# Performance work log

Measured on AMD Instinct MI355X. Metric: run time of the kernel, lower is better.

## Reference

```python
import jax, jax.numpy as jnp
import numpy as np

B, T, E, H, D_PRICE = 16, 2048, 128, 4, 512


def setup_inputs() -> dict:
    key = jax.random.key(0)
    ks = jax.random.split(key, 22)
    f32 = jnp.float32

    def w(k, shape):
        fan_in = shape[0]
        return (jax.random.normal(k, shape, f32) / np.sqrt(fan_in)).astype(f32)

    def b(k, n):
        return (jax.random.normal(k, (n,), f32) * 0.01).astype(f32)

    inp = {
        # OHLC prices, positive, normalized scale
        "ohlc": jax.random.uniform(ks[0], (B, T, 4), f32, 0.5, 1.5),
        # ohlc_proj: Linear(4, 64)
        "Wp": w(ks[1], (4, 64)), "bp": b(ks[2], 64),
        # curvature_net: Linear(64,128) -> ReLU -> Linear(128,32)
        "Wc1": w(ks[3], (64, 128)), "bc1": b(ks[4], 128),
        "Wc2": w(ks[5], (128, 32)), "bc2": b(ks[6], 32),
        # volatility_net: Linear(64,64) -> ReLU -> Linear(64,16)
        "Wv1": w(ks[7], (64, 64)), "bv1": b(ks[8], 64),
        "Wv2": w(ks[9], (64, 16)), "bv2": b(ks[10], 16),
        # sr_field_net: Linear(64,64) -> ReLU -> Linear(64,16)
        "Ws1": w(ks[11], (64, 64)), "bs1": b(ks[12], 64),
        "Ws2": w(ks[13], (64, 16)), "bs2": b(ks[14], 16),
        # MultiheadAttention(embed_dim=128, num_heads=4): fused in-proj + out-proj
        "Wqkv": w(ks[15], (E, 3 * E)), "bqkv": b(ks[16], 3 * E),
        "Wo": w(ks[17], (E, E)), "bo": b(ks[18], E),
        # output_proj: Linear(128, d_price)
        "Wout": w(ks[19], (E, D_PRICE)), "bout": b(ks[20], D_PRICE),
    }
    return inp


def _mlp(x, W1, b1, W2, b2):
    return jax.nn.relu(x @ W1 + b1) @ W2 + b2


def reference(ohlc, Wp, bp, Wc1, bc1, Wc2, bc2, Wv1, bv1, Wv2, bv2,
              Ws1, bs1, Ws2, bs2, Wqkv, bqkv, Wo, bo, Wout, bout):
    # NB: compute_curvature / compute_volatility_surface / detect_sr_levels
    # in the original forward are dead code (results never used), so they are
    # omitted here; output math is identical.
    e = ohlc @ Wp + bp                                   # [B,T,64]
    feats = jnp.concatenate([
        e,
        _mlp(e, Wc1, bc1, Wc2, bc2),                     # [B,T,32]
        _mlp(e, Wv1, bv1, Wv2, bv2),                     # [B,T,16]
        _mlp(e, Ws1, bs1, Ws2, bs2),                     # [B,T,16]
    ], axis=-1)                                          # [B,T,128]

    Bn, Tn, En = feats.shape
    dh = En // H
    qkv = feats @ Wqkv + bqkv                            # [B,T,3E]
    q, k, v = jnp.split(qkv, 3, axis=-1)

    def heads(x):
        return x.reshape(Bn, Tn, H, dh).transpose(0, 2, 1, 3)  # [B,H,T,dh]

    q, k, v = heads(q), heads(k), heads(v)
    scores = jnp.einsum('bhqd,bhkd->bhqk', q, k) / np.sqrt(dh).astype(feats.dtype)
    a = jax.nn.softmax(scores, axis=-1)                  # [B,H,T,T]
    o = jnp.einsum('bhqk,bhkd->bhqd', a, v)
    o = o.transpose(0, 2, 1, 3).reshape(Bn, Tn, En)
    attended = o @ Wo + bo                               # [B,T,128]

    pooled = attended.mean(axis=1)                       # [B,128]
    return pooled @ Wout + bout                          # [B,512]
```

## Files before the change

### kernel.cpp

```cpp
#include <hip/hip_runtime.h>


typedef __attribute__((ext_vector_type(4)))  float f32x4;
typedef __attribute__((ext_vector_type(4)))  short short4v;
typedef __attribute__((ext_vector_type(8)))  short short8v;

static __device__ __forceinline__ unsigned short f2b(float f) {
    unsigned int u = __builtin_bit_cast(unsigned int, f);
    u += 0x7fffu + ((u >> 16) & 1u);
    return (unsigned short)(u >> 16);
}

static __device__ __forceinline__ unsigned int cvtpk_bf16(float a, float b) {
    unsigned int r;
    asm volatile("v_cvt_pk_bf16_f32 %0, %1, %2" : "=v"(r) : "v"(a), "v"(b));
    return r;
}

__global__ __launch_bounds__(256) void prep_kernel(
    const float* Wqkv, const float* Wc1, const float* Wc2, const float* Wv1,
    const float* Wv2, const float* Ws1, const float* Ws2,
    unsigned short* wqkvt, unsigned short* wc1t, unsigned short* wc2t,
    unsigned short* wv1t, unsigned short* wv2t, unsigned short* ws1t,
    unsigned short* ws2t, float* pooled, float* qkmax)
{
    int tid = threadIdx.x;
    if (blockIdx.x < 48) {
        __shared__ float tile[32][33];
        int bidn = blockIdx.x % 12, bidk = blockIdx.x / 12;
        int n0 = bidn * 32, k0 = bidk * 32;
        {
            int r = tid >> 3, cq = tid & 7;
            float4 v = *(const float4*)(Wqkv + (size_t)(k0 + r) * 384 + n0 + cq * 4);
            tile[r][cq*4+0] = v.x; tile[r][cq*4+1] = v.y;
            tile[r][cq*4+2] = v.z; tile[r][cq*4+3] = v.w;
        }
        __syncthreads();
        {
            int nr = tid >> 3, kq = tid & 7;
            union { unsigned short us[4]; short4v v; } pk;
#pragma unroll
            for (int j = 0; j < 4; ++j) pk.us[j] = f2b(tile[kq*4+j][nr]);
            *(short4v*)(wqkvt + (size_t)(n0 + nr) * 128 + k0 + kq * 4) = pk.v;
        }
        return;
    }
    int idx = (blockIdx.x - 48) * 256 + tid;
    if (idx < 8192)  { int n = idx >> 6, kk = idx & 63;  wc1t[idx] = f2b(Wc1[kk*128 + n]); return; }
    idx -= 8192;
    if (idx < 4096)  { int n = idx >> 7, kk = idx & 127; wc2t[idx] = f2b(Wc2[kk*32  + n]); return; }
    idx -= 4096;
    if (idx < 4096)  { int n = idx >> 6, kk = idx & 63;  wv1t[idx] = f2b(Wv1[kk*64  + n]); return; }
    idx -= 4096;
    if (idx < 1024)  { int n = idx >> 6, kk = idx & 63;  wv2t[idx] = f2b(Wv2[kk*16  + n]); return; }
    idx -= 1024;
    if (idx < 4096)  { int n = idx >> 6, kk = idx & 63;  ws1t[idx] = f2b(Ws1[kk*64  + n]); return; }
    idx -= 4096;
    if (idx < 1024)  { int n = idx >> 6, kk = idx & 63;  ws2t[idx] = f2b(Ws2[kk*16  + n]); return; }
    idx -= 1024;
    if (idx < 2048)  { pooled[idx] = 0.f; return; }
    idx -= 2048;
    if (idx < 128)   qkmax[idx] = 0.f;
}

template<int N, int K, int A_ROWB, int D_ROWB, bool RELU, bool TO_LDS>
static __device__ __forceinline__ void tile_gemm(
    const char* As, const unsigned short* __restrict__ BT,
    const float* __restrict__ bias, char* dst,
    unsigned short* __restrict__ gOut, int ocol,
    int m0, int w, int lane)
{
    constexpr int ASL = A_ROWB / 16, DSL = D_ROWB / 16;
    constexpr int NT = N / 16, KS = K / 32;
    int l15 = lane & 15, hi4 = lane >> 4;
    f32x4 acc[NT];
#pragma unroll
    for (int nt = 0; nt < NT; ++nt)
#pragma unroll
        for (int r = 0; r < 4; ++r) acc[nt][r] = 0.f;

#pragma unroll
    for (int ks = 0; ks < KS; ++ks) {
        int slot = ks * 4 + hi4;
        int m = w * 16 + l15;
        short8v af = *(const short8v*)(As + m * A_ROWB + ((slot ^ (m & (ASL - 1))) << 4));
#pragma unroll
        for (int nt = 0; nt < NT; ++nt) {
            int n = nt * 16 + l15;
            short8v bf = *(const short8v*)(BT + (size_t)n * K + slot * 8);
            acc[nt] = __builtin_amdgcn_mfma_f32_16x16x32_bf16(af, bf, acc[nt], 0, 0, 0);
        }
    }
#pragma unroll
    for (int nt = 0; nt < NT; ++nt) {
        int n = nt * 16 + l15;
        float bv = bias[n];
#pragma unroll
        for (int r = 0; r < 4; ++r) {
            int m = w * 16 + hi4 * 4 + r;
            float v = acc[nt][r] + bv;
            if (RELU) v = fmaxf(v, 0.f);
            if (TO_LDS) {
                int col = n;
                *(unsigned short*)(dst + m * D_ROWB + (((col >> 3) ^ (m & (DSL - 1))) << 4) + (col & 7) * 2) = f2b(v);
            } else {
                gOut[(size_t)(m0 + m) * 128 + ocol + n] = f2b(v);
            }
        }
    }
}

__global__ __launch_bounds__(256) void fused_mlp(
    const float* __restrict__ ohlc, const float* __restrict__ Wp, const float* __restrict__ bp,
    const unsigned short* __restrict__ wc1t, const float* __restrict__ bc1,
    const unsigned short* __restrict__ wc2t, const float* __restrict__ bc2,
    const unsigned short* __restrict__ wv1t, const float* __restrict__ bv1,
    const unsigned short* __restrict__ wv2t, const float* __restrict__ bv2,
    const unsigned short* __restrict__ ws1t, const float* __restrict__ bs1,
    const unsigned short* __restrict__ ws2t, const float* __restrict__ bs2,
    unsigned short* __restrict__ feats)
{
    __shared__ float wp[256];
    __shared__ float bpl[64];
    __shared__ char Et[64 * 128];
    __shared__ char Hc[64 * 256];
    __shared__ char Hv[64 * 128];
    __shared__ char Hs[64 * 128];

    int tid = threadIdx.x;
    int m0 = blockIdx.x * 64;
    wp[tid] = Wp[tid];
    if (tid < 64) bpl[tid] = bp[tid];
    __syncthreads();

    {
        int tok = tid >> 2, jq = tid & 3;
        float4 ov = ((const float4*)ohlc)[m0 + tok];
#pragma unroll
        for (int c = 0; c < 2; ++c) {
            int sl = jq * 2 + c;
            union { unsigned short us[8]; short8v v; } pk;
#pragma unroll
            for (int jj = 0; jj < 8; ++jj) {
                int j = sl * 8 + jj;
                float e = bpl[j] + ov.x * wp[j] + ov.y * wp[64 + j]
                                 + ov.z * wp[128 + j] + ov.w * wp[192 + j];
                pk.us[jj] = f2b(e);
            }
            *(short8v*)(Et + tok * 128 + ((sl ^ (tok & 7)) << 4)) = pk.v;
            *(short8v*)(feats + (size_t)(m0 + tok) * 128 + sl * 8) = pk.v;
        }
    }
    __syncthreads();

    int lane = tid & 63, w = tid >> 6;
    tile_gemm<128, 64, 128, 256, true, true >(Et, wc1t, bc1, Hc, feats, 0, m0, w, lane);
    tile_gemm< 64, 64, 128, 128, true, true >(Et, wv1t, bv1, Hv, feats, 0, m0, w, lane);
    tile_gemm< 64, 64, 128, 128, true, true >(Et, ws1t, bs1, Hs, feats, 0, m0, w, lane);
    tile_gemm< 32, 128, 256, 256, false, false>(Hc, wc2t, bc2, Hc, feats, 64,  m0, w, lane);
    tile_gemm< 16,  64, 128, 128, false, false>(Hv, wv2t, bv2, Hv, feats, 96,  m0, w, lane);
    tile_gemm< 16,  64, 128, 128, false, false>(Hs, ws2t, bs2, Hs, feats, 112, m0, w, lane);
}

__global__ __launch_bounds__(256) void qkv_gemm(
    const unsigned short* __restrict__ feats,
    const unsigned short* __restrict__ wqkvt, const float* __restrict__ bqkv,
    unsigned short* __restrict__ qg, unsigned short* __restrict__ kg,
    unsigned short* __restrict__ vt2, float* __restrict__ qkmax)
{
    constexpr int ROWB = 256, CPR = 16;
    __shared__ short8v smemv[4096];
    char* As = (char*)smemv;
    char* Bs = (char*)smemv + 32768;

    int tid = threadIdx.x;
    int m0 = blockIdx.x * 128;
    int sel = blockIdx.y;
    const unsigned short* BT = wqkvt + (size_t)sel * 128 * 128;

    for (int c = tid; c < 128 * CPR; c += 256) {
        int m = c / CPR, s = c % CPR;
        short8v v = *(const short8v*)(feats + (size_t)(m0 + m) * 128 + s * 8);
        *(short8v*)(As + m * ROWB + ((s ^ (m & 15)) * 16)) = v;
    }
    for (int c = tid; c < 128 * CPR; c += 256) {
        int n = c / CPR, s = c % CPR;
        short8v v = *(const short8v*)(BT + (size_t)n * 128 + s * 8);
        *(short8v*)(Bs + n * ROWB + ((s ^ (n & 15)) * 16)) = v;
    }
    __syncthreads();

    int lane = tid & 63, w = tid >> 6;
    int l15 = lane & 15, hi4 = lane >> 4;

    f32x4 acc[2][8];
#pragma unroll
    for (int mt = 0; mt < 2; ++mt)
#pragma unroll
        for (int nt = 0; nt < 8; ++nt)
#pragma unroll
            for (int r = 0; r < 4; ++r) acc[mt][nt][r] = 0.f;

#pragma unroll
    for (int ks = 0; ks < 4; ++ks) {
        int slot = ks * 4 + hi4;
        short8v af[2];
#pragma unroll
        for (int mt = 0; mt < 2; ++mt) {
            int m = w * 32 + mt * 16 + l15;
            af[mt] = *(const short8v*)(As + m * ROWB + ((slot ^ (m & 15)) * 16));
        }
#pragma unroll
        for (int nt = 0; nt < 8; ++nt) {
            int n = nt * 16 + l15;
            short8v bf = *(const short8v*)(Bs + n * ROWB + ((slot ^ (n & 15)) * 16));
            acc[0][nt] = __builtin_amdgcn_mfma_f32_16x16x32_bf16(af[0], bf, acc[0][nt], 0, 0, 0);
            acc[1][nt] = __builtin_amdgcn_mfma_f32_16x16x32_bf16(af[1], bf, acc[1][nt], 0, 0, 0);
        }
    }

    const float QSCALE = 1.4426950408889634f * 0.17677669529663687f;
    int b = m0 >> 11, tp0 = m0 & 2047;

    if (sel == 2) {
#pragma unroll
        for (int mt = 0; mt < 2; ++mt)
#pragma unroll
            for (int nt = 0; nt < 8; ++nt) {
                int n = nt * 16 + l15;
                float bv = bqkv[256 + n];
                int h = n >> 5, dh = n & 31;
                uint2 pk;
                pk.x = cvtpk_bf16(acc[mt][nt][0] + bv, acc[mt][nt][1] + bv);
                pk.y = cvtpk_bf16(acc[mt][nt][2] + bv, acc[mt][nt][3] + bv);
                int g32 = (tp0 >> 5) + w;
                size_t o = (size_t)(b * 4 + h) * 65536 + (size_t)g32 * 1024
                         + dh * 32 + hi4 * 8 + mt * 4;
                *(uint2*)(vt2 + o) = pk;
            }
    } else {
        float amax[4] = {0.f, 0.f, 0.f, 0.f};
        float scale = (sel == 0) ? QSCALE : 1.0f;
#pragma unroll
        for (int mt = 0; mt < 2; ++mt)
#pragma unroll
            for (int nt = 0; nt < 8; ++nt) {
                int n = nt * 16 + l15;
                float bv = bqkv[sel * 128 + n];
#pragma unroll
                for (int r = 0; r < 4; ++r) {
                    float v = (acc[mt][nt][r] + bv) * scale;
                    amax[nt >> 1] = fmaxf(amax[nt >> 1], fabsf(v));
                    int m = w * 32 + mt * 16 + hi4 * 4 + r;
                    *(unsigned short*)(As + m * 256 + (((n >> 3) ^ (m & 7)) << 4) + (n & 7) * 2) = f2b(v);
                }
            }
#pragma unroll
        for (int g = 0; g < 4; ++g) {
            float mv = amax[g];
            mv = fmaxf(mv, __shfl_xor(mv, 1));  mv = fmaxf(mv, __shfl_xor(mv, 2));
            mv = fmaxf(mv, __shfl_xor(mv, 4));  mv = fmaxf(mv, __shfl_xor(mv, 8));
            mv = fmaxf(mv, __shfl_xor(mv, 16)); mv = fmaxf(mv, __shfl_xor(mv, 32));
            if (lane == 0)
                atomicMax((int*)(qkmax + sel * 64 + b * 4 + g), __float_as_int(mv));
        }
        __syncthreads();
        unsigned short* og = (sel == 0) ? qg : kg;
#pragma unroll
        for (int it = 0; it < 8; ++it) {
            int ch = it * 256 + tid;
            int m = ch >> 4, c = ch & 15;
            short8v vv = *(const short8v*)(As + m * 256 + ((c ^ (m & 7)) << 4));
            int h = c >> 2, dq = c & 3;
            *(short8v*)(og + ((size_t)(b * 4 + h) * 2048 + tp0 + m) * 32 + dq * 8) = vv;
        }
    }
}

__global__ __launch_bounds__(512) void attn_kernel(
    const unsigned short* __restrict__ qg, const unsigned short* __restrict__ kg,
    const unsigned short* __restrict__ vt2, const float* __restrict__ qkmax,
    float* __restrict__ pooled)
{
    __shared__ char Kv[2][4096];

    int tid = threadIdx.x, bid = blockIdx.x;
    int bh = bid & 63, qc = bid >> 6;
    int b = bh >> 2;
    int lane = tid & 63, w = tid >> 6;
    int l15 = lane & 15, h = (lane >> 4) & 3;
    int q0 = qc * 256 + w * 32;

    const char* qp = (const char*)qg + ((size_t)bh * 2048 + q0) * 64 + l15 * 64 + h * 16;
    short8v Qf[2];
    Qf[0] = *(const short8v*)(qp);
    Qf[1] = *(const short8v*)(qp + 1024);

    float negM0 = -(32.0f * qkmax[bh] * qkmax[64 + bh]);
    f32x4 NEGM4 = {negM0, negM0, negM0, negM0};

    f32x4 accO[2][2], lacc[2];
#pragma unroll
    for (int j = 0; j < 2; ++j)
#pragma unroll
        for (int r = 0; r < 4; ++r) { accO[j][0][r] = 0.f; accO[j][1][r] = 0.f; lacc[j][r] = 0.f; }

    short8v ONES;
    {
        union { unsigned short us[8]; short8v v; } u;
#pragma unroll
        for (int j = 0; j < 8; ++j) u.us[j] = 0x3F80;
        ONES = u.v;
    }

    const char* gk = (const char*)kg  + (size_t)bh * 131072;
    const char* gv = (const char*)vt2 + (size_t)bh * 131072;
    const char* gsrc = (tid < 256) ? (gk + (tid & 255) * 8) : (gv + (tid & 255) * 8);
    int ldst = (tid < 256) ? (tid * 8) : (2048 + (tid - 256) * 8);
    int foff = l15 * 64 + h * 16;

    auto compute = [&](const char* bufp) {
        short8v Ka = *(const short8v*)(bufp + foff);
        short8v Kb = *(const short8v*)(bufp + 1024 + foff);
        short8v Va = *(const short8v*)(bufp + 2048 + foff);
        short8v Vb = *(const short8v*)(bufp + 3072 + foff);
        union { unsigned int u[4]; short8v v; } pk[2];
#pragma unroll
        for (int tau = 0; tau < 2; ++tau) {
            short8v Kf = tau ? Kb : Ka;
#pragma unroll
            for (int j = 0; j < 2; ++j) {
                f32x4 s = __builtin_amdgcn_mfma_f32_16x16x32_bf16(Kf, Qf[j], NEGM4, 0, 0, 0);
                float p0 = __builtin_amdgcn_exp2f(s[0]);
                float p1 = __builtin_amdgcn_exp2f(s[1]);
                float p2 = __builtin_amdgcn_exp2f(s[2]);
                float p3 = __builtin_amdgcn_exp2f(s[3]);
                pk[j].u[tau * 2 + 0] = cvtpk_bf16(p0, p1);
                pk[j].u[tau * 2 + 1] = cvtpk_bf16(p2, p3);
            }
        }
#pragma unroll
        for (int j = 0; j < 2; ++j) {
            lacc[j]    = __builtin_amdgcn_mfma_f32_16x16x32_bf16(ONES, pk[j].v, lacc[j], 0, 0, 0);
            accO[j][0] = __builtin_amdgcn_mfma_f32_16x16x32_bf16(Va,   pk[j].v, accO[j][0], 0, 0, 0);
            accO[j][1] = __builtin_amdgcn_mfma_f32_16x16x32_bf16(Vb,   pk[j].v, accO[j][1], 0, 0, 0);
        }
    };

    uint2 R;
    R = *(const uint2*)(gsrc);
    *(uint2*)(Kv[0] + ldst) = R;
    R = *(const uint2*)(gsrc + 2048);
    __syncthreads();

#pragma unroll 1
    for (int g = 0; g < 64; g += 2) {
        *(uint2*)(Kv[1] + ldst) = R;
        if (g + 2 < 64) R = *(const uint2*)(gsrc + (size_t)(g + 2) * 2048);
        compute(Kv[0]);
        __syncthreads();
        if (g + 2 < 64) *(uint2*)(Kv[0] + ldst) = R;
        if (g + 3 < 64) R = *(const uint2*)(gsrc + (size_t)(g + 3) * 2048);
        compute(Kv[1]);
        __syncthreads();
    }

    float o8[2][4];
#pragma unroll
    for (int d = 0; d < 2; ++d)
#pragma unroll
        for (int r = 0; r < 4; ++r) o8[d][r] = 0.f;
#pragma unroll
    for (int j = 0; j < 2; ++j) {
        float inv = 1.0f / (lacc[j][0] + 1e-30f);
#pragma unroll
        for (int d = 0; d < 2; ++d)
#pragma unroll
            for (int r = 0; r < 4; ++r) o8[d][r] += accO[j][d][r] * inv;
    }
#pragma unroll
    for (int d = 0; d < 2; ++d)
#pragma unroll
        for (int r = 0; r < 4; ++r) {
            float v = o8[d][r];
            v += __shfl_xor(v, 1); v += __shfl_xor(v, 2);
            v += __shfl_xor(v, 4); v += __shfl_xor(v, 8);
            if (l15 == 0) {
                int dh = d * 16 + h * 4 + r;
                atomicAdd(pooled + b * 128 + (bh & 3) * 32 + dh, v);
            }
        }
}

__global__ __launch_bounds__(256) void head_kernel(
    const float* __restrict__ pooled, const float* __restrict__ Wo,
    const float* __restrict__ bo, const float* __restrict__ Wout,
    const float* __restrict__ bout, float* __restrict__ out)
{
    int bq = blockIdx.x, tid = threadIdx.x;
    __shared__ float pl[128], mid[128];
    if (tid < 128) pl[tid] = pooled[bq * 128 + tid] * (1.f / 2048.f);
    __syncthreads();
    if (tid < 128) {
        float s = bo[tid];
#pragma unroll 4
        for (int c = 0; c < 128; ++c) s += pl[c] * Wo[c * 128 + tid];
        mid[tid] = s;
    }
    __syncthreads();
    for (int j = tid; j < 512; j += 256) {
        float s = bout[j];
#pragma unroll 4
        for (int i = 0; i < 128; ++i) s += mid[i] * Wout[i * 512 + j];
        out[bq * 512 + j] = s;
    }
}

extern "C" void kernel_launch(void* const* d_in, const int* in_sizes, int n_in,
                              void* d_out, int out_size, void* d_ws, size_t ws_size,
                              hipStream_t stream) {
    (void)in_sizes; (void)n_in; (void)out_size; (void)ws_size;
    const float* ohlc = (const float*)d_in[0];
    const float* Wp   = (const float*)d_in[1];  const float* bp   = (const float*)d_in[2];
    const float* Wc1  = (const float*)d_in[3];  const float* bc1  = (const float*)d_in[4];
    const float* Wc2  = (const float*)d_in[5];  const float* bc2  = (const float*)d_in[6];
    const float* Wv1  = (const float*)d_in[7];  const float* bv1  = (const float*)d_in[8];
    const float* Wv2  = (const float*)d_in[9];  const float* bv2  = (const float*)d_in[10];
    const float* Ws1  = (const float*)d_in[11]; const float* bs1  = (const float*)d_in[12];
    const float* Ws2  = (const float*)d_in[13]; const float* bs2  = (const float*)d_in[14];
    const float* Wqkv = (const float*)d_in[15]; const float* bqkv = (const float*)d_in[16];
    const float* Wo   = (const float*)d_in[17]; const float* bo   = (const float*)d_in[18];
    const float* Wout = (const float*)d_in[19]; const float* bout = (const float*)d_in[20];
    float* out = (float*)d_out;
    char* ws = (char*)d_ws;

    const size_t MB8 = 8388608;
    unsigned short* feats = (unsigned short*)(ws);
    unsigned short* qg    = (unsigned short*)(ws + 1 * MB8);
    unsigned short* kg    = (unsigned short*)(ws + 2 * MB8);
    unsigned short* vt2   = (unsigned short*)(ws + 3 * MB8);
    float*          pooled = (float*)(ws + 4 * MB8);
    float*          qkmax  = (float*)(ws + 4 * MB8 + 8192);
    unsigned short* wc1t  = (unsigned short*)(ws + 4 * MB8 + 8192 + 512);
    unsigned short* wc2t  = wc1t + 8192;
    unsigned short* wv1t  = wc2t + 4096;
    unsigned short* wv2t  = wv1t + 4096;
    unsigned short* ws1t  = wv2t + 1024;
    unsigned short* ws2t  = ws1t + 4096;
    unsigned short* wqkvt = ws2t + 1024;

    prep_kernel<<<145, 256, 0, stream>>>(Wqkv, Wc1, Wc2, Wv1, Wv2, Ws1, Ws2,
                                         wqkvt, wc1t, wc2t, wv1t, wv2t, ws1t, ws2t,
                                         pooled, qkmax);
    fused_mlp<<<512, 256, 0, stream>>>(ohlc, Wp, bp, wc1t, bc1, wc2t, bc2,
                                       wv1t, bv1, wv2t, bv2, ws1t, bs1, ws2t, bs2, feats);
    qkv_gemm<<<dim3(256, 3), 256, 0, stream>>>(feats, wqkvt, bqkv, qg, kg, vt2, qkmax);
    attn_kernel<<<512, 512, 0, stream>>>(qg, kg, vt2, qkmax, pooled);
    head_kernel<<<16, 256, 0, stream>>>(pooled, Wo, bo, Wout, bout, out);
}
```

Baseline: 131.4 us.

## Split MLP branches across grid and halve attention block size

The fused MLP kernel now launches three blocks per token tile, one per branch (curvature, volatility, S/R), with one shared hidden buffer instead of three. This shrinks shared memory per block and triples the block count, at the cost of recomputing the OHLC projection three times. The attention kernel moves from 512-thread blocks covering 256 queries to 256-thread blocks covering 128 queries. Each thread now loads 16 bytes of K/V per step instead of 8, which doubles the number of blocks and gives the scheduler finer granularity, but makes each block re-stream K/V for fewer queries.

```diff
diff --git a/kernel.cpp b/kernel.cpp
--- a/kernel.cpp
+++ b/kernel.cpp
@@ -123,12 +123,11 @@
     __shared__ float wp[256];
     __shared__ float bpl[64];
     __shared__ char Et[64 * 128];
-    __shared__ char Hc[64 * 256];
-    __shared__ char Hv[64 * 128];
-    __shared__ char Hs[64 * 128];
+    __shared__ char Ht[64 * 256];
 
     int tid = threadIdx.x;
     int m0 = blockIdx.x * 64;
+    int branch = blockIdx.y;
     wp[tid] = Wp[tid];
     if (tid < 64) bpl[tid] = bp[tid];
     __syncthreads();
@@ -148,18 +147,23 @@
                 pk.us[jj] = f2b(e);
             }
             *(short8v*)(Et + tok * 128 + ((sl ^ (tok & 7)) << 4)) = pk.v;
-            *(short8v*)(feats + (size_t)(m0 + tok) * 128 + sl * 8) = pk.v;
+            if (branch == 0)
+                *(short8v*)(feats + (size_t)(m0 + tok) * 128 + sl * 8) = pk.v;
         }
     }
     __syncthreads();
 
     int lane = tid & 63, w = tid >> 6;
-    tile_gemm<128, 64, 128, 256, true, true >(Et, wc1t, bc1, Hc, feats, 0, m0, w, lane);
-    tile_gemm< 64, 64, 128, 128, true, true >(Et, wv1t, bv1, Hv, feats, 0, m0, w, lane);
-    tile_gemm< 64, 64, 128, 128, true, true >(Et, ws1t, bs1, Hs, feats, 0, m0, w, lane);
-    tile_gemm< 32, 128, 256, 256, false, false>(Hc, wc2t, bc2, Hc, feats, 64,  m0, w, lane);
-    tile_gemm< 16,  64, 128, 128, false, false>(Hv, wv2t, bv2, Hv, feats, 96,  m0, w, lane);
-    tile_gemm< 16,  64, 128, 128, false, false>(Hs, ws2t, bs2, Hs, feats, 112, m0, w, lane);
+    if (branch == 0) {
+        tile_gemm<128, 64, 128, 256, true, true >(Et, wc1t, bc1, Ht, feats, 0,  m0, w, lane);
+        tile_gemm< 32, 128, 256, 256, false, false>(Ht, wc2t, bc2, Ht, feats, 64, m0, w, lane);
+    } else if (branch == 1) {
+        tile_gemm< 64, 64, 128, 128, true, true >(Et, wv1t, bv1, Ht, feats, 0,  m0, w, lane);
+        tile_gemm< 16, 64, 128, 128, false, false>(Ht, wv2t, bv2, Ht, feats, 96, m0, w, lane);
+    } else {
+        tile_gemm< 64, 64, 128, 128, true, true >(Et, ws1t, bs1, Ht, feats, 0,   m0, w, lane);
+        tile_gemm< 16, 64, 128, 128, false, false>(Ht, ws2t, bs2, Ht, feats, 112, m0, w, lane);
+    }
 }
 
 __global__ __launch_bounds__(256) void qkv_gemm(
@@ -277,7 +281,7 @@
     }
 }
 
-__global__ __launch_bounds__(512) void attn_kernel(
+__global__ __launch_bounds__(256) void attn_kernel(
     const unsigned short* __restrict__ qg, const unsigned short* __restrict__ kg,
     const unsigned short* __restrict__ vt2, const float* __restrict__ qkmax,
     float* __restrict__ pooled)
@@ -289,7 +293,7 @@
     int b = bh >> 2;
     int lane = tid & 63, w = tid >> 6;
     int l15 = lane & 15, h = (lane >> 4) & 3;
-    int q0 = qc * 256 + w * 32;
+    int q0 = qc * 128 + w * 32;
 
     const char* qp = (const char*)qg + ((size_t)bh * 2048 + q0) * 64 + l15 * 64 + h * 16;
     short8v Qf[2];
@@ -315,8 +319,8 @@
 
     const char* gk = (const char*)kg  + (size_t)bh * 131072;
     const char* gv = (const char*)vt2 + (size_t)bh * 131072;
-    const char* gsrc = (tid < 256) ? (gk + (tid & 255) * 8) : (gv + (tid & 255) * 8);
-    int ldst = (tid < 256) ? (tid * 8) : (2048 + (tid - 256) * 8);
+    const char* gsrc = (tid < 128) ? (gk + tid * 16) : (gv + (tid - 128) * 16);
+    int ldst = tid * 16;
     int foff = l15 * 64 + h * 16;
 
     auto compute = [&](const char* bufp) {
@@ -347,20 +351,20 @@
         }
     };
 
-    uint2 R;
-    R = *(const uint2*)(gsrc);
-    *(uint2*)(Kv[0] + ldst) = R;
-    R = *(const uint2*)(gsrc + 2048);
+    short8v R;
+    R = *(const short8v*)(gsrc);
+    *(short8v*)(Kv[0] + ldst) = R;
+    R = *(const short8v*)(gsrc + 2048);
     __syncthreads();
 
 #pragma unroll 1
     for (int g = 0; g < 64; g += 2) {
-        *(uint2*)(Kv[1] + ldst) = R;
-        if (g + 2 < 64) R = *(const uint2*)(gsrc + (size_t)(g + 2) * 2048);
+        *(short8v*)(Kv[1] + ldst) = R;
+        if (g + 2 < 64) R = *(const short8v*)(gsrc + (size_t)(g + 2) * 2048);
         compute(Kv[0]);
         __syncthreads();
-        if (g + 2 < 64) *(uint2*)(Kv[0] + ldst) = R;
-        if (g + 3 < 64) R = *(const uint2*)(gsrc + (size_t)(g + 3) * 2048);
+        if (g + 2 < 64) *(short8v*)(Kv[0] + ldst) = R;
+        if (g + 3 < 64) R = *(const short8v*)(gsrc + (size_t)(g + 3) * 2048);
         compute(Kv[1]);
         __syncthreads();
     }
@@ -452,9 +456,9 @@
     prep_kernel<<<145, 256, 0, stream>>>(Wqkv, Wc1, Wc2, Wv1, Wv2, Ws1, Ws2,
                                          wqkvt, wc1t, wc2t, wv1t, wv2t, ws1t, ws2t,
                                          pooled, qkmax);
-    fused_mlp<<<512, 256, 0, stream>>>(ohlc, Wp, bp, wc1t, bc1, wc2t, bc2,
-                                       wv1t, bv1, wv2t, bv2, ws1t, bs1, ws2t, bs2, feats);
+    fused_mlp<<<dim3(512, 3), 256, 0, stream>>>(ohlc, Wp, bp, wc1t, bc1, wc2t, bc2,
+                                                wv1t, bv1, wv2t, bv2, ws1t, bs1, ws2t, bs2, feats);
     qkv_gemm<<<dim3(256, 3), 256, 0, stream>>>(feats, wqkvt, bqkv, qg, kg, vt2, qkmax);
-    attn_kernel<<<512, 512, 0, stream>>>(qg, kg, vt2, qkmax, pooled);
+    attn_kernel<<<1024, 256, 0, stream>>>(qg, kg, vt2, qkmax, pooled);
     head_kernel<<<16, 256, 0, stream>>>(pooled, Wo, bo, Wout, bout, out);
 }
```

New measurement: 134.7 us. 1.03x slower.
